# Optimization experiments

Hardware: AMD Instinct MI355X
Metric: run time of the kernel (lower is better)

The kernel has to match this reference:

```python
import jax, jax.numpy as jnp
import numpy as np


def setup_inputs() -> dict:
    key = jax.random.key(0)
    k1, k2, k3 = jax.random.split(key, 3)
    bs, n1, n2, d1, d2, dout = 4, 128, 128, 768, 768, 768
    input1 = jax.random.normal(k1, (bs, n1, d1), dtype=jnp.float32)
    input2 = jax.random.normal(k2, (bs, n2, d2), dtype=jnp.float32)
    # torch Linear(sum_dims, dout): we store W as (d1+d2, dout) so y = x @ W + b
    W = jax.random.normal(k3, (d1 + d2, dout), dtype=jnp.float32) * (1.0 / np.sqrt(d1 + d2))
    b = jnp.zeros((dout,), dtype=jnp.float32)
    return {"input1": input1, "input2": input2, "W": W, "b": b}


def reference(input1, input2, W, b):
    # Original: expand to [bs,n1,n2,d1]/[bs,n1,n2,d2], cat -> [bs,n1,n2,d1+d2], Linear.
    # Algebraically identical without materializing the concat:
    #   cat([x1,x2]) @ W = x1 @ W[:d1] + x2 @ W[d1:]
    d1 = input1.shape[-1]
    W1, W2 = W[:d1], W[d1:]
    p1 = jnp.einsum("bnd,do->bno", input1, W1)  # [bs, n1, dout]
    p2 = jnp.einsum("bmd,do->bmo", input2, W2)  # [bs, n2, dout]
    # broadcast-sum over the pair grid -> [bs, n1, n2, dout]
    return p1[:, :, None, :] + p2[:, None, :, :] + b
```

## Files before the change

kernel.cpp:

```cpp
#include <hip/hip_runtime.h>

typedef float f4    __attribute__((ext_vector_type(4)));
typedef float f32x4 __attribute__((ext_vector_type(4)));
typedef short short8 __attribute__((ext_vector_type(8)));
typedef unsigned short u16x4 __attribute__((ext_vector_type(4)));

#define NCHUNK 24

__device__ inline unsigned short f2bf(float x) {
    union { float f; unsigned u; } v; v.f = x;
    return (unsigned short)((v.u + 0x7FFFu + ((v.u >> 16) & 1u)) >> 16);
}
__device__ inline float bf2f(unsigned short h) {
    union { unsigned u; float f; } v; v.u = ((unsigned)h) << 16;
    return v.f;
}

__global__ __launch_bounds__(512) void fused_kernel(
    const float* __restrict__ A1, const float* __restrict__ A2,
    const float* __restrict__ W, const float* __restrict__ bias,
    float* __restrict__ out)
{
    __shared__ union {
        struct {
            unsigned short Ah[4096], Al[4096], Bh[4096], Bl[4096];
        } s;
        float p[128][68];
    } u;

    const int o0 = blockIdx.x * 64;
    const int nm = blockIdx.y;
    const int b  = nm >> 2;
    const int n0 = ((nm >> 1) & 1) * 64;
    const int m0 = (nm & 1) * 64;
    const int t    = threadIdx.x;
    const int lane = t & 63;
    const int w    = t >> 6;

    const float* aptr[2]; int a_dst[2];
    #pragma unroll
    for (int q = 0; q < 2; ++q) {
        const int a  = t + q * 512;
        const int rc = a >> 3;
        const int k0 = (a & 7) * 4;
        const float* base = (rc < 64)
            ? (A1 + (size_t)(b * 128 + n0 + rc) * 768)
            : (A2 + (size_t)(b * 128 + m0 + (rc - 64)) * 768);
        aptr[q]  = base + k0;
        a_dst[q] = (rc >> 4) * 512 + (k0 >> 3) * 128 + (rc & 15) * 8 + (k0 & 7);
    }
    const float* bptr[2]; int b_dst[2];
    #pragma unroll
    for (int q = 0; q < 2; ++q) {
        const int v  = t + q * 512;
        const int oc = v & 127;
        const int kk = (v >> 7) * 4;
        const int z  = oc >> 6;
        bptr[q]  = W + (size_t)(z * 768 + kk) * 768 + (o0 + (oc & 63));
        b_dst[q] = (oc >> 4) * 512 + (kk >> 3) * 128 + (oc & 15) * 8 + (kk & 7);
    }

    f4 rA[2]; float rB[2][4];
    #pragma unroll
    for (int q = 0; q < 2; ++q) {
        rA[q] = *(const f4*)(aptr[q]);
        #pragma unroll
        for (int j = 0; j < 4; ++j) rB[q][j] = bptr[q][(size_t)j * 768];
    }

    f32x4 acc[4] = {0, 0, 0, 0};

    for (int c = 0; c < NCHUNK; ++c) {
        #pragma unroll
        for (int q = 0; q < 2; ++q) {
            u16x4 h, l;
            #pragma unroll
            for (int j = 0; j < 4; ++j) {
                h[j] = f2bf(rA[q][j]);
                l[j] = f2bf(rA[q][j] - bf2f(h[j]));
            }
            *(u16x4*)&u.s.Ah[a_dst[q]] = h;
            *(u16x4*)&u.s.Al[a_dst[q]] = l;
        }
        #pragma unroll
        for (int q = 0; q < 2; ++q) {
            u16x4 h, l;
            #pragma unroll
            for (int j = 0; j < 4; ++j) {
                h[j] = f2bf(rB[q][j]);
                l[j] = f2bf(rB[q][j] - bf2f(h[j]));
            }
            *(u16x4*)&u.s.Bh[b_dst[q]] = h;
            *(u16x4*)&u.s.Bl[b_dst[q]] = l;
        }
        __syncthreads();

        if (c + 1 < NCHUNK) {
            const int k0 = (c + 1) * 32;
            #pragma unroll
            for (int q = 0; q < 2; ++q) {
                rA[q] = *(const f4*)(aptr[q] + k0);
                #pragma unroll
                for (int j = 0; j < 4; ++j)
                    rB[q][j] = bptr[q][(size_t)(k0 + j) * 768];
            }
        }

        {
            const short8 ah = *(const short8*)&u.s.Ah[w * 512 + lane * 8];
            const short8 al = *(const short8*)&u.s.Al[w * 512 + lane * 8];
            const int bt0 = (w >> 2) * 4;
            #pragma unroll
            for (int ct = 0; ct < 4; ++ct) {
                const short8 bh = *(const short8*)&u.s.Bh[(bt0 + ct) * 512 + lane * 8];
                const short8 bl = *(const short8*)&u.s.Bl[(bt0 + ct) * 512 + lane * 8];
                acc[ct] = __builtin_amdgcn_mfma_f32_16x16x32_bf16(ah, bh, acc[ct], 0, 0, 0);
                acc[ct] = __builtin_amdgcn_mfma_f32_16x16x32_bf16(ah, bl, acc[ct], 0, 0, 0);
                acc[ct] = __builtin_amdgcn_mfma_f32_16x16x32_bf16(al, bh, acc[ct], 0, 0, 0);
            }
        }
        __syncthreads();
    }

    #pragma unroll
    for (int ct = 0; ct < 4; ++ct)
        #pragma unroll
        for (int i = 0; i < 4; ++i)
            u.p[w * 16 + (lane >> 4) * 4 + i][ct * 16 + (lane & 15)] = acc[ct][i];
    __syncthreads();

    const int o4 = (t & 15) * 4;
    const int nn = t >> 4;
    const f4 bb  = *(const f4*)(bias + o0 + o4);
    const f4 p1a = *(const f4*)&u.p[nn * 2 + 0][o4] + bb;
    const f4 p1b = *(const f4*)&u.p[nn * 2 + 1][o4] + bb;

    float* ob = out + ((size_t)(b * 128 + n0 + nn * 2) * 128 + m0) * 768 + o0 + o4;
    const size_t nstride = (size_t)128 * 768;

    #pragma unroll 4
    for (int m = 0; m < 64; ++m) {
        const f4 p2v = *(const f4*)&u.p[64 + m][o4];
        __builtin_nontemporal_store(p1a + p2v, (f4*)(ob + (size_t)m * 768));
        __builtin_nontemporal_store(p1b + p2v, (f4*)(ob + nstride + (size_t)m * 768));
    }
}

extern "C" void kernel_launch(void* const* d_in, const int* in_sizes, int n_in,
                              void* d_out, int out_size, void* d_ws, size_t ws_size,
                              hipStream_t stream)
{
    const float* input1 = (const float*)d_in[0];
    const float* input2 = (const float*)d_in[1];
    const float* W      = (const float*)d_in[2];
    const float* bias   = (const float*)d_in[3];
    float* out = (float*)d_out;

    fused_kernel<<<dim3(12, 16), 512, 0, stream>>>(input1, input2, W, bias, out);
}
```

Measured before the change: 268.3 us.

## Precompute bf16 hi/lo split into workspace and double-buffer MFMA tiles

Adds a separate conversion kernel that splits the fp32 inputs and weights into bf16 high/low pairs once, writing them into the workspace already in MFMA tile layout. The GEMM kernel then streams these pre-swizzled tiles with vector loads into double-buffered LDS, using one sync per chunk. This removes the redundant per-block conversion and the strided scalar loads of W, at the cost of an extra launch and workspace traffic. The old fused kernel remains as a fallback when the workspace is too small.

```diff
diff --git a/kernel.cpp b/kernel.cpp
--- a/kernel.cpp
+++ b/kernel.cpp
@@ -3,28 +3,167 @@
 typedef float f4    __attribute__((ext_vector_type(4)));
 typedef float f32x4 __attribute__((ext_vector_type(4)));
 typedef short short8 __attribute__((ext_vector_type(8)));
+typedef unsigned short u16;
 typedef unsigned short u16x4 __attribute__((ext_vector_type(4)));
 
 #define NCHUNK 24
 
-__device__ inline unsigned short f2bf(float x) {
+#define AWS_U16 1572864u
+#define WWS_U16 2359296u
+
+__device__ inline u16 f2bf(float x) {
     union { float f; unsigned u; } v; v.f = x;
-    return (unsigned short)((v.u + 0x7FFFu + ((v.u >> 16) & 1u)) >> 16);
-}
-__device__ inline float bf2f(unsigned short h) {
+    return (u16)((v.u + 0x7FFFu + ((v.u >> 16) & 1u)) >> 16);
+}
+__device__ inline float bf2f(u16 h) {
     union { unsigned u; float f; } v; v.u = ((unsigned)h) << 16;
     return v.f;
 }
 
-__global__ __launch_bounds__(512) void fused_kernel(
+__global__ __launch_bounds__(512) void convert_kernel(
+    const float* __restrict__ A1, const float* __restrict__ A2,
+    const float* __restrict__ W, u16* __restrict__ Aws, u16* __restrict__ Wws)
+{
+    const int id = blockIdx.x * 512 + threadIdx.x;
+    if (blockIdx.x < 384) {
+        const int u   = id;
+        const int row = u / 192;
+        const int k   = (u - row * 192) * 4;
+        const float* src = (row < 512) ? (A1 + (size_t)row * 768 + k)
+                                       : (A2 + (size_t)(row - 512) * 768 + k);
+        const f4 v = *(const f4*)src;
+        u16x4 h, l;
+        #pragma unroll
+        for (int j = 0; j < 4; ++j) { h[j] = f2bf(v[j]); l[j] = f2bf(v[j] - bf2f(h[j])); }
+        const int g = row >> 6, rt = (row >> 4) & 3, r = row & 15;
+        const int c = k >> 5, kq = (k >> 3) & 3, ki0 = k & 7;
+        const size_t base = (size_t)g * 98304 + c * 4096 + rt * 512 + kq * 128 + r * 8 + ki0;
+        *(u16x4*)&Aws[base]        = h;
+        *(u16x4*)&Aws[base + 2048] = l;
+    } else {
+        const int u   = id - 384 * 512;
+        const int o   = u % 768;
+        const int kk4 = u / 768;
+        const int kk  = kk4 * 4;
+        const int z   = (kk4 >= 192);
+        const int k   = kk - z * 768;
+        u16x4 h, l;
+        #pragma unroll
+        for (int j = 0; j < 4; ++j) {
+            const float v = W[(size_t)(kk + j) * 768 + o];
+            h[j] = f2bf(v); l[j] = f2bf(v - bf2f(h[j]));
+        }
+        const int rt = o >> 4, r = o & 15;
+        const int c = k >> 5, kq = (k >> 3) & 3, ki0 = k & 7;
+        const size_t base = (size_t)c * 98304 + (size_t)z * 49152
+                          + rt * 512 + kq * 128 + r * 8 + ki0;
+        *(u16x4*)&Wws[base]         = h;
+        *(u16x4*)&Wws[base + 24576] = l;
+    }
+}
+
+__global__ __launch_bounds__(512) void mfma_ws_kernel(
+    const u16* __restrict__ Aws, const u16* __restrict__ Wws,
+    const float* __restrict__ bias, float* __restrict__ out)
+{
+    __shared__ union {
+        u16   st[2][16384];
+        float p[128][68];
+    } u;
+
+    const int o0 = blockIdx.x * 64;
+    const int nm = blockIdx.y;
+    const int b  = nm >> 2, hn = (nm >> 1) & 1, hm = nm & 1;
+    const int n0 = hn * 64, m0 = hm * 64;
+    const int g_n = b * 2 + hn;
+    const int g_m = 8 + b * 2 + hm;
+    const int t = threadIdx.x, lane = t & 63, w = t >> 6;
+    const int rt0 = blockIdx.x * 4;
+    const int r2  = t >> 8;
+    const int t8  = (t & 255) * 8;
+
+    const u16* sA1 = Aws + (size_t)g_n * 98304 + t * 8;
+    const u16* sA2 = Aws + (size_t)g_m * 98304 + t * 8;
+    const u16* sW1 = Wws + (size_t)r2 * 24576 + rt0 * 512 + t8;
+    const u16* sW2 = sW1 + 49152;
+
+    f4 rA1 = *(const f4*)(sA1);
+    f4 rA2 = *(const f4*)(sA2);
+    f4 rW1 = *(const f4*)(sW1);
+    f4 rW2 = *(const f4*)(sW2);
+    *(f4*)&u.st[0][t * 8]                  = rA1;
+    *(f4*)&u.st[0][4096 + t * 8]           = rA2;
+    *(f4*)&u.st[0][8192 + r2 * 2048 + t8]  = rW1;
+    *(f4*)&u.st[0][12288 + r2 * 2048 + t8] = rW2;
+    __syncthreads();
+
+    f32x4 acc[4] = {0, 0, 0, 0};
+
+    for (int c = 0; c < NCHUNK; ++c) {
+        const int s = c & 1;
+        if (c + 1 < NCHUNK) {
+            rA1 = *(const f4*)(sA1 + (size_t)(c + 1) * 4096);
+            rA2 = *(const f4*)(sA2 + (size_t)(c + 1) * 4096);
+            rW1 = *(const f4*)(sW1 + (size_t)(c + 1) * 98304);
+            rW2 = *(const f4*)(sW2 + (size_t)(c + 1) * 98304);
+        }
+        {
+            const u16* S  = u.st[s];
+            const u16* ab = (w < 4) ? (S + w * 512) : (S + 4096 + (w - 4) * 512);
+            const short8 ah = *(const short8*)(ab + lane * 8);
+            const short8 al = *(const short8*)(ab + 2048 + lane * 8);
+            const u16* Bb = (w < 4) ? (S + 8192) : (S + 12288);
+            #pragma unroll
+            for (int ct = 0; ct < 4; ++ct) {
+                const short8 bh = *(const short8*)(Bb + ct * 512 + lane * 8);
+                const short8 bl = *(const short8*)(Bb + 2048 + ct * 512 + lane * 8);
+                acc[ct] = __builtin_amdgcn_mfma_f32_16x16x32_bf16(ah, bh, acc[ct], 0, 0, 0);
+                acc[ct] = __builtin_amdgcn_mfma_f32_16x16x32_bf16(ah, bl, acc[ct], 0, 0, 0);
+                acc[ct] = __builtin_amdgcn_mfma_f32_16x16x32_bf16(al, bh, acc[ct], 0, 0, 0);
+            }
+        }
+        if (c + 1 < NCHUNK) {
+            const int ns = s ^ 1;
+            *(f4*)&u.st[ns][t * 8]                  = rA1;
+            *(f4*)&u.st[ns][4096 + t * 8]           = rA2;
+            *(f4*)&u.st[ns][8192 + r2 * 2048 + t8]  = rW1;
+            *(f4*)&u.st[ns][12288 + r2 * 2048 + t8] = rW2;
+            __syncthreads();
+        }
+    }
+    __syncthreads();
+
+    #pragma unroll
+    for (int ct = 0; ct < 4; ++ct)
+        #pragma unroll
+        for (int i = 0; i < 4; ++i)
+            u.p[w * 16 + (lane >> 4) * 4 + i][ct * 16 + (lane & 15)] = acc[ct][i];
+    __syncthreads();
+
+    const int o4 = (t & 15) * 4;
+    const int nn = t >> 4;
+    const f4 bb  = *(const f4*)(bias + o0 + o4);
+    const f4 p1a = *(const f4*)&u.p[nn * 2 + 0][o4] + bb;
+    const f4 p1b = *(const f4*)&u.p[nn * 2 + 1][o4] + bb;
+
+    float* ob = out + ((size_t)(b * 128 + n0 + nn * 2) * 128 + m0) * 768 + o0 + o4;
+    const size_t nstride = (size_t)128 * 768;
+
+    #pragma unroll 4
+    for (int m = 0; m < 64; ++m) {
+        const f4 p2v = *(const f4*)&u.p[64 + m][o4];
+        __builtin_nontemporal_store(p1a + p2v, (f4*)(ob + (size_t)m * 768));
+        __builtin_nontemporal_store(p1b + p2v, (f4*)(ob + nstride + (size_t)m * 768));
+    }
+}
+
+__global__ __launch_bounds__(512) void fused_v6(
     const float* __restrict__ A1, const float* __restrict__ A2,
     const float* __restrict__ W, const float* __restrict__ bias,
     float* __restrict__ out)
 {
     __shared__ union {
-        struct {
-            unsigned short Ah[4096], Al[4096], Bh[4096], Bl[4096];
-        } s;
+        struct { u16 Ah[4096], Al[4096], Bh[4096], Bl[4096]; } s;
         float p[128][68];
     } u;
 
@@ -33,30 +172,22 @@
     const int b  = nm >> 2;
     const int n0 = ((nm >> 1) & 1) * 64;
     const int m0 = (nm & 1) * 64;
-    const int t    = threadIdx.x;
-    const int lane = t & 63;
-    const int w    = t >> 6;
+    const int t = threadIdx.x, lane = t & 63, w = t >> 6;
 
     const float* aptr[2]; int a_dst[2];
     #pragma unroll
     for (int q = 0; q < 2; ++q) {
-        const int a  = t + q * 512;
-        const int rc = a >> 3;
-        const int k0 = (a & 7) * 4;
-        const float* base = (rc < 64)
-            ? (A1 + (size_t)(b * 128 + n0 + rc) * 768)
-            : (A2 + (size_t)(b * 128 + m0 + (rc - 64)) * 768);
-        aptr[q]  = base + k0;
+        const int a = t + q * 512, rc = a >> 3, k0 = (a & 7) * 4;
+        const float* base = (rc < 64) ? (A1 + (size_t)(b * 128 + n0 + rc) * 768)
+                                      : (A2 + (size_t)(b * 128 + m0 + (rc - 64)) * 768);
+        aptr[q] = base + k0;
         a_dst[q] = (rc >> 4) * 512 + (k0 >> 3) * 128 + (rc & 15) * 8 + (k0 & 7);
     }
     const float* bptr[2]; int b_dst[2];
     #pragma unroll
     for (int q = 0; q < 2; ++q) {
-        const int v  = t + q * 512;
-        const int oc = v & 127;
-        const int kk = (v >> 7) * 4;
-        const int z  = oc >> 6;
-        bptr[q]  = W + (size_t)(z * 768 + kk) * 768 + (o0 + (oc & 63));
+        const int v = t + q * 512, oc = v & 127, kk = (v >> 7) * 4, z = oc >> 6;
+        bptr[q] = W + (size_t)(z * 768 + kk) * 768 + (o0 + (oc & 63));
         b_dst[q] = (oc >> 4) * 512 + (kk >> 3) * 128 + (oc & 15) * 8 + (kk & 7);
     }
 
@@ -69,43 +200,31 @@
     }
 
     f32x4 acc[4] = {0, 0, 0, 0};
-
     for (int c = 0; c < NCHUNK; ++c) {
         #pragma unroll
         for (int q = 0; q < 2; ++q) {
             u16x4 h, l;
             #pragma unroll
-            for (int j = 0; j < 4; ++j) {
-                h[j] = f2bf(rA[q][j]);
-                l[j] = f2bf(rA[q][j] - bf2f(h[j]));
-            }
-            *(u16x4*)&u.s.Ah[a_dst[q]] = h;
-            *(u16x4*)&u.s.Al[a_dst[q]] = l;
+            for (int j = 0; j < 4; ++j) { h[j] = f2bf(rA[q][j]); l[j] = f2bf(rA[q][j] - bf2f(h[j])); }
+            *(u16x4*)&u.s.Ah[a_dst[q]] = h; *(u16x4*)&u.s.Al[a_dst[q]] = l;
         }
         #pragma unroll
         for (int q = 0; q < 2; ++q) {
             u16x4 h, l;
             #pragma unroll
-            for (int j = 0; j < 4; ++j) {
-                h[j] = f2bf(rB[q][j]);
-                l[j] = f2bf(rB[q][j] - bf2f(h[j]));
-            }
-            *(u16x4*)&u.s.Bh[b_dst[q]] = h;
-            *(u16x4*)&u.s.Bl[b_dst[q]] = l;
+            for (int j = 0; j < 4; ++j) { h[j] = f2bf(rB[q][j]); l[j] = f2bf(rB[q][j] - bf2f(h[j])); }
+            *(u16x4*)&u.s.Bh[b_dst[q]] = h; *(u16x4*)&u.s.Bl[b_dst[q]] = l;
         }
         __syncthreads();
-
         if (c + 1 < NCHUNK) {
             const int k0 = (c + 1) * 32;
             #pragma unroll
             for (int q = 0; q < 2; ++q) {
                 rA[q] = *(const f4*)(aptr[q] + k0);
                 #pragma unroll
-                for (int j = 0; j < 4; ++j)
-                    rB[q][j] = bptr[q][(size_t)(k0 + j) * 768];
+                for (int j = 0; j < 4; ++j) rB[q][j] = bptr[q][(size_t)(k0 + j) * 768];
             }
         }
-
         {
             const short8 ah = *(const short8*)&u.s.Ah[w * 512 + lane * 8];
             const short8 al = *(const short8*)&u.s.Al[w * 512 + lane * 8];
@@ -121,7 +240,6 @@
         }
         __syncthreads();
     }
-
     #pragma unroll
     for (int ct = 0; ct < 4; ++ct)
         #pragma unroll
@@ -129,15 +247,12 @@
             u.p[w * 16 + (lane >> 4) * 4 + i][ct * 16 + (lane & 15)] = acc[ct][i];
     __syncthreads();
 
-    const int o4 = (t & 15) * 4;
-    const int nn = t >> 4;
+    const int o4 = (t & 15) * 4, nn = t >> 4;
     const f4 bb  = *(const f4*)(bias + o0 + o4);
     const f4 p1a = *(const f4*)&u.p[nn * 2 + 0][o4] + bb;
     const f4 p1b = *(const f4*)&u.p[nn * 2 + 1][o4] + bb;
-
     float* ob = out + ((size_t)(b * 128 + n0 + nn * 2) * 128 + m0) * 768 + o0 + o4;
     const size_t nstride = (size_t)128 * 768;
-
     #pragma unroll 4
     for (int m = 0; m < 64; ++m) {
         const f4 p2v = *(const f4*)&u.p[64 + m][o4];
@@ -156,5 +271,14 @@
     const float* bias   = (const float*)d_in[3];
     float* out = (float*)d_out;
 
-    fused_kernel<<<dim3(12, 16), 512, 0, stream>>>(input1, input2, W, bias, out);
-}
+    const size_t need = (size_t)(AWS_U16 + WWS_U16) * sizeof(u16);
+
+    if (ws_size >= need) {
+        u16* Aws = (u16*)d_ws;
+        u16* Wws = Aws + AWS_U16;
+        convert_kernel<<<dim3(960), 512, 0, stream>>>(input1, input2, W, Aws, Wws);
+        mfma_ws_kernel<<<dim3(12, 16), 512, 0, stream>>>(Aws, Wws, bias, out);
+    } else {
+        fused_v6<<<dim3(12, 16), 512, 0, stream>>>(input1, input2, W, bias, out);
+    }
+}
```

Result: faster. 243.3 us (-9.3%).
